# Performance work log

Hardware: AMD Instinct MI355X
Metric: run time of the kernel (lower is better)

The kernel has to match this reference:

```python
import jax, jax.numpy as jnp
import numpy as np

LN_EPS = 1e-5
SCALE = 1.0 / 8.0  # 1/sqrt(dim/num_heads) = 1/sqrt(64)


def layernorm(x, g, b):
    m = jnp.mean(x, axis=-1, keepdims=True)
    v = jnp.mean(jnp.square(x - m), axis=-1, keepdims=True)
    return (x - m) * jax.lax.rsqrt(v + LN_EPS) * g + b


def attention_block(q_in, kv_in, wq, bq, wk, bk, wv, bv, g, b):
    # un-split single-matrix attention, faithful to the source (no head reshape)
    Q = q_in @ wq + bq            # [B,S,D]
    K = kv_in @ wk + bk           # [B,T,D]
    V = kv_in @ wv + bv           # [B,T,D]
    scores = jnp.einsum('bsd,btd->bst', Q, K) * SCALE  # [B,S,T]
    A = jax.nn.softmax(scores, axis=-1)
    out = jnp.einsum('bst,btd->bsd', A, V)
    return layernorm(out + q_in, g, b)


def setup_inputs() -> dict:
    key = jax.random.key(0)
    ks = jax.random.split(key, 16)
    B, S, T, D = 4, 2048, 2048, 1024
    w = lambda k: jax.random.normal(k, (D, D), dtype=jnp.float32) * 0.02
    z = jnp.zeros((D,), dtype=jnp.float32)
    o = jnp.ones((D,), dtype=jnp.float32)
    return {
        'x': jax.random.normal(ks[0], (B, S, D), dtype=jnp.float32),
        'y': jax.random.normal(ks[1], (B, T, D), dtype=jnp.float32),
        'wq_m': w(ks[2]), 'bq_m': z, 'wk_m': w(ks[3]), 'bk_m': z,
        'wv_m': w(ks[4]), 'bv_m': z, 'g_m': o, 'b_m': z,
        'wq_c': w(ks[5]), 'bq_c': z, 'wk_c': w(ks[6]), 'bk_c': z,
        'wv_c': w(ks[7]), 'bv_c': z, 'g_c': o, 'b_c': z,
        'f0_w': w(ks[8]), 'f0_b': z, 'f1_w': w(ks[9]), 'f1_b': z,
        'g_d': o, 'b_d': z,
    }


def reference(x, y,
              wq_m, bq_m, wk_m, bk_m, wv_m, bv_m, g_m, b_m,
              wq_c, bq_c, wk_c, bk_c, wv_c, bv_c, g_c, b_c,
              f0_w, f0_b, f1_w, f1_b, g_d, b_d):
    # masked (self) attention + shared decoder LN residual
    res = x
    x = layernorm(attention_block(x, x, wq_m, bq_m, wk_m, bk_m, wv_m, bv_m, g_m, b_m) + res, g_d, b_d)
    # cross attention against memory y
    res = x
    x = layernorm(attention_block(x, y, wq_c, bq_c, wk_c, bk_c, wv_c, bv_c, g_c, b_c) + res, g_d, b_d)
    # FFN: loop condition in source is always true -> GELU (exact) after every layer
    res = x
    x = jax.nn.gelu(x @ f0_w + f0_b, approximate=False)
    x = jax.nn.gelu(x @ f1_w + f1_b, approximate=False)
    return layernorm(x + res, g_d, b_d)
```

## Files before the change

### kernel.cpp

```cpp
#include <hip/hip_runtime.h>

#define DEV __device__ __forceinline__

typedef __attribute__((ext_vector_type(8))) short bf16x8;
typedef __attribute__((ext_vector_type(4))) float f32x4;

DEV float bf2f(unsigned short u) { return __uint_as_float(((unsigned int)u) << 16); }
DEV unsigned short f2bf(float f) {
    unsigned int x = __float_as_uint(f);
    return (unsigned short)((x + 0x7fffu + ((x >> 16) & 1u)) >> 16);
}
DEV float gelu_exact(float x) { return 0.5f * x * (1.0f + erff(x * 0.7071067811865475f)); }

DEV void gload16(const void* g, void* l) {
    __builtin_amdgcn_global_load_lds((const __attribute__((address_space(1))) void*)g,
                                     (__attribute__((address_space(3))) void*)l, 16, 0, 0);
}

template <int OFF>
DEV bf16x8 ds_read128(unsigned addr) {
    bf16x8 r;
    asm volatile("ds_read_b128 %0, %1 offset:%2" : "=v"(r) : "v"(addr), "i"(OFF));
    return r;
}

struct WPtrs { const float* p[8]; };

__global__ __launch_bounds__(256) void transpose_cast_w8(WPtrs wp,
                                                         unsigned short* __restrict__ out,
                                                         int R, int C) {
    const float* in = wp.p[blockIdx.z];
    out += (size_t)blockIdx.z * R * C;
    __shared__ float tile[32][33];
    int c0 = blockIdx.x * 32, r0 = blockIdx.y * 32;
    int tx = threadIdx.x, ty = threadIdx.y;
#pragma unroll
    for (int i = 0; i < 32; i += 8)
        tile[ty + i][tx] = in[(size_t)(r0 + ty + i) * C + (c0 + tx)];
    __syncthreads();
#pragma unroll
    for (int i = 0; i < 32; i += 8)
        out[(size_t)(c0 + ty + i) * R + (r0 + tx)] = f2bf(tile[tx][ty + i]);
}

__global__ __launch_bounds__(256) void cast_f32_bf16(const float* __restrict__ in,
                                                     unsigned short* __restrict__ out, int n4) {
    int i = blockIdx.x * 256 + threadIdx.x;
    if (i >= n4) return;
    float4 v = ((const float4*)in)[i];
    unsigned short o[4] = {f2bf(v.x), f2bf(v.y), f2bf(v.z), f2bf(v.w)};
    *(uint2*)(out + (size_t)i * 4) = *(uint2*)o;
}


template <int H>
DEV void mfma16q(const bf16x8 (&a)[2][2], const bf16x8 (&b)[4][2], f32x4 (&acc)[4][4]) {
#pragma unroll
    for (int ks = 0; ks < 2; ++ks)
#pragma unroll
        for (int n = 0; n < 4; ++n) {
            acc[2 * H][n]     = __builtin_amdgcn_mfma_f32_16x16x32_bf16(a[0][ks], b[n][ks], acc[2 * H][n], 0, 0, 0);
            acc[2 * H + 1][n] = __builtin_amdgcn_mfma_f32_16x16x32_bf16(a[1][ks], b[n][ks], acc[2 * H + 1][n], 0, 0, 0);
        }
}

template <int BIAS_MODE, bool GELU_ACT, bool OUT_F32>
__global__ __launch_bounds__(256, 2) void gemm128(const unsigned short* __restrict__ A,
                                                  const unsigned short* __restrict__ BT,
                                                  const float* __restrict__ bias,
                                                  const float* __restrict__ biasB,
                                                  float* __restrict__ Cf,
                                                  unsigned short* __restrict__ Cb,
                                                  int N, int K, int lda, int ldb, float scale,
                                                  long sA, long sB, long sC) {
    const int gx = gridDim.x, gy = gridDim.y;
    int f = blockIdx.x + gx * (blockIdx.y + gy * blockIdx.z);
    const int nwg = gx * gy * gridDim.z;
    f = (f & 7) * (nwg >> 3) + (f >> 3);
    const int bz = f / (gx * gy);
    const int rem = f - bz * gx * gy;
    const int by = rem / gx;
    const int bx = rem - by * gx;

    A += (long)bz * sA;
    BT += (long)bz * sB;
    if (BIAS_MODE == 1 && biasB != nullptr && bz == 1) bias = biasB;

    const int tid = threadIdx.x;
    const int lane = tid & 63;
    const int wave = tid >> 6;
    const int wr = wave >> 1;
    const int wc = wave & 1;
    const int llo = lane & 15, lhi = lane >> 4;
    const int bm = bx * 128, bn = by * 128;

    __shared__ unsigned short lds[2][2][128 * 64];

    const int xk0 = (0 + lhi) ^ (llo & 7);
    const int xk1 = (4 + lhi) ^ (llo & 7);

    const unsigned base0 = (unsigned)(size_t)&lds[0][0][0];
    const unsigned aA0 = base0 + (unsigned)(wr * 64 + llo) * 128u + xk0 * 16;
    const unsigned aA1 = base0 + (unsigned)(wr * 64 + llo) * 128u + xk1 * 16;
    const unsigned aB0 = base0 + (unsigned)(wc * 64 + llo) * 128u + xk0 * 16;
    const unsigned aB1 = base0 + (unsigned)(wc * 64 + llo) * 128u + xk1 * 16;

    int srow[4], sq[4];
#pragma unroll
    for (int L = 0; L < 4; ++L) {
        const int d = L * 256 + tid;
        srow[L] = d >> 3;
        sq[L] = (d & 7) ^ (srow[L] & 7);
    }
    const unsigned short* gA = A + (size_t)bm * lda;
    const unsigned short* gB = BT + (size_t)bn * ldb;

#define SA(kt, BUF)                                                                     \
    {                                                                                   \
        _Pragma("unroll") for (int L = 0; L < 4; ++L)                                   \
            gload16(gA + (size_t)srow[L] * lda + (kt) + sq[L] * 8,                      \
                    &lds[BUF][0][(L * 256 + wave * 64) * 8]);                           \
    }
#define SB(kt, BUF)                                                                     \
    {                                                                                   \
        _Pragma("unroll") for (int L = 0; L < 4; ++L)                                   \
            gload16(gB + (size_t)srow[L] * ldb + (kt) + sq[L] * 8,                      \
                    &lds[BUF][1][(L * 256 + wave * 64) * 8]);                           \
    }

    f32x4 acc[4][4] = {};
    bf16x8 b[4][2];

#define PH(H, BUF, LOADB, STG, TAIL)                                         \
    {                                                                        \
        STG;                                                                 \
        bf16x8 afr[2][2];                                                    \
        afr[0][0] = ds_read128<(BUF)*32768 + (H)*4096 + 0>(aA0);             \
        afr[0][1] = ds_read128<(BUF)*32768 + (H)*4096 + 0>(aA1);             \
        afr[1][0] = ds_read128<(BUF)*32768 + (H)*4096 + 2048>(aA0);          \
        afr[1][1] = ds_read128<(BUF)*32768 + (H)*4096 + 2048>(aA1);          \
        if (LOADB) {                                                         \
            b[0][0] = ds_read128<(BUF)*32768 + 16384 + 0>(aB0);              \
            b[0][1] = ds_read128<(BUF)*32768 + 16384 + 0>(aB1);              \
            b[1][0] = ds_read128<(BUF)*32768 + 16384 + 2048>(aB0);           \
            b[1][1] = ds_read128<(BUF)*32768 + 16384 + 2048>(aB1);           \
            b[2][0] = ds_read128<(BUF)*32768 + 16384 + 4096>(aB0);           \
            b[2][1] = ds_read128<(BUF)*32768 + 16384 + 4096>(aB1);           \
            b[3][0] = ds_read128<(BUF)*32768 + 16384 + 6144>(aB0);           \
            b[3][1] = ds_read128<(BUF)*32768 + 16384 + 6144>(aB1);           \
        }                                                                    \
        __builtin_amdgcn_s_barrier();                                        \
        asm volatile("s_waitcnt lgkmcnt(0)" :::);                            \
        __builtin_amdgcn_sched_barrier(0);                                   \
        __builtin_amdgcn_s_setprio(1);                                       \
        mfma16q<H>(afr, b, acc);                                             \
        __builtin_amdgcn_s_setprio(0);                                       \
        TAIL;                                                                \
        __builtin_amdgcn_s_barrier();                                        \
    }

#define VM0 asm volatile("s_waitcnt vmcnt(0)" :::)
#define NOP ((void)0)

    const int nt = K >> 6;

    SA(0, 0);
    SB(0, 0);
    VM0;
    __builtin_amdgcn_s_barrier();

    int kt = 0;
    for (int t = 0; t < nt; t += 2) {
        const bool st0 = (t + 1 < nt);
        const bool st1 = (t + 2 < nt);
        PH(0, 0, true,  if (st0) { SA(kt + 64, 1); SB(kt + 64, 1); }, NOP);
        PH(1, 0, false, NOP, VM0);
        PH(0, 1, true,  if (st1) { SA(kt + 128, 0); SB(kt + 128, 0); }, NOP);
        PH(1, 1, false, NOP, VM0);
        kt += 128;
    }
#undef PH
#undef SA
#undef SB
#undef VM0
#undef NOP

#pragma unroll
    for (int m = 0; m < 4; ++m) {
#pragma unroll
        for (int n = 0; n < 4; ++n) {
            const int col = bn + wc * 64 + n * 16 + llo;
            float bcol = 0.f;
            if constexpr (BIAS_MODE == 1) bcol = bias[col];
#pragma unroll
            for (int j = 0; j < 4; ++j) {
                const int row = bm + wr * 64 + m * 16 + lhi * 4 + j;
                float v = acc[m][n][j] * scale + bcol;
                if constexpr (BIAS_MODE == 2) v += bias[row];
                if constexpr (GELU_ACT) v = gelu_exact(v);
                const size_t idx = (size_t)bz * (size_t)sC + (size_t)row * N + col;
                if constexpr (OUT_F32) Cf[idx] = v;
                else Cb[idx] = f2bf(v);
            }
        }
    }
}

__global__ __launch_bounds__(256) void softmax_rows(unsigned short* __restrict__ s, int T) {
    __shared__ float red[4];
    unsigned short* p = s + (size_t)blockIdx.x * T;
    const int tid = threadIdx.x;

    uint4 raw = *(const uint4*)(p + tid * 8);
    const unsigned short* u = (const unsigned short*)&raw;
    float v[8];
#pragma unroll
    for (int j = 0; j < 8; ++j) v[j] = bf2f(u[j]);

    float mx = -3.4e38f;
#pragma unroll
    for (int j = 0; j < 8; ++j) mx = fmaxf(mx, v[j]);
#pragma unroll
    for (int o = 32; o; o >>= 1) mx = fmaxf(mx, __shfl_xor(mx, o));
    if ((tid & 63) == 0) red[tid >> 6] = mx;
    __syncthreads();
    mx = fmaxf(fmaxf(red[0], red[1]), fmaxf(red[2], red[3]));
    __syncthreads();

    float sum = 0.f;
#pragma unroll
    for (int j = 0; j < 8; ++j) {
        v[j] = expf(v[j] - mx);
        sum += v[j];
    }
#pragma unroll
    for (int o = 32; o; o >>= 1) sum += __shfl_xor(sum, o);
    if ((tid & 63) == 0) red[tid >> 6] = sum;
    __syncthreads();
    sum = red[0] + red[1] + red[2] + red[3];
    const float inv = 1.0f / sum;

    unsigned short o8[8];
#pragma unroll
    for (int j = 0; j < 8; ++j) o8[j] = f2bf(v[j] * inv);
    *(uint4*)(p + tid * 8) = *(uint4*)o8;
}

DEV float block_sum(float v, float* red, int tid) {
#pragma unroll
    for (int o = 32; o; o >>= 1) v += __shfl_xor(v, o);
    if ((tid & 63) == 0) red[tid >> 6] = v;
    __syncthreads();
    v = red[0] + red[1] + red[2] + red[3];
    __syncthreads();
    return v;
}

__global__ __launch_bounds__(256) void ln_double(const unsigned short* __restrict__ av,
                                                 const float* __restrict__ xin,
                                                 const float* __restrict__ g1, const float* __restrict__ b1,
                                                 const float* __restrict__ g2, const float* __restrict__ b2,
                                                 float* __restrict__ xout,
                                                 unsigned short* __restrict__ xbf, int D) {
    __shared__ float red[4];
    const int tid = threadIdx.x;
    const size_t base = (size_t)blockIdx.x * D + tid * 4;
    uint2 a2 = *(const uint2*)(av + base);
    const unsigned short* au = (const unsigned short*)&a2;
    const float4 x4 = *(const float4*)(xin + base);
    float x[4] = {x4.x, x4.y, x4.z, x4.w};
    float t[4];
#pragma unroll
    for (int j = 0; j < 4; ++j) t[j] = bf2f(au[j]) + x[j];
    const float invD = 1.0f / D;

    float m = block_sum(t[0] + t[1] + t[2] + t[3], red, tid) * invD;
    float q = 0.f;
#pragma unroll
    for (int j = 0; j < 4; ++j) q += (t[j] - m) * (t[j] - m);
    q = block_sum(q, red, tid) * invD;
    float rs = rsqrtf(q + 1e-5f);

    float u[4];
#pragma unroll
    for (int j = 0; j < 4; ++j) {
        const int idx = tid * 4 + j;
        u[j] = (t[j] - m) * rs * g1[idx] + b1[idx] + x[j];
    }
    float m2 = block_sum(u[0] + u[1] + u[2] + u[3], red, tid) * invD;
    float q2 = 0.f;
#pragma unroll
    for (int j = 0; j < 4; ++j) q2 += (u[j] - m2) * (u[j] - m2);
    q2 = block_sum(q2, red, tid) * invD;
    float rs2 = rsqrtf(q2 + 1e-5f);

    float4 o4;
    unsigned short ob[4];
#pragma unroll
    for (int j = 0; j < 4; ++j) {
        const int idx = tid * 4 + j;
        float o = (u[j] - m2) * rs2 * g2[idx] + b2[idx];
        ((float*)&o4)[j] = o;
        ob[j] = f2bf(o);
    }
    *(float4*)(xout + base) = o4;
    *(uint2*)(xbf + base) = *(uint2*)ob;
}

__global__ __launch_bounds__(256) void ln_single(const unsigned short* __restrict__ a,
                                                 const float* __restrict__ b_,
                                                 const float* __restrict__ g, const float* __restrict__ bb,
                                                 float* __restrict__ out, int D) {
    __shared__ float red[4];
    const int tid = threadIdx.x;
    const size_t base = (size_t)blockIdx.x * D + tid * 4;
    uint2 a2 = *(const uint2*)(a + base);
    const unsigned short* au = (const unsigned short*)&a2;
    const float4 x4 = *(const float4*)(b_ + base);
    float t[4] = {bf2f(au[0]) + x4.x, bf2f(au[1]) + x4.y, bf2f(au[2]) + x4.z, bf2f(au[3]) + x4.w};
    const float invD = 1.0f / D;
    float m = block_sum(t[0] + t[1] + t[2] + t[3], red, tid) * invD;
    float q = 0.f;
#pragma unroll
    for (int j = 0; j < 4; ++j) q += (t[j] - m) * (t[j] - m);
    q = block_sum(q, red, tid) * invD;
    float rs = rsqrtf(q + 1e-5f);
    float4 o4;
#pragma unroll
    for (int j = 0; j < 4; ++j) {
        const int idx = tid * 4 + j;
        ((float*)&o4)[j] = (t[j] - m) * rs * g[idx] + bb[idx];
    }
    *(float4*)(out + base) = o4;
}

extern "C" void kernel_launch(void* const* d_in, const int* in_sizes, int n_in,
                              void* d_out, int out_size, void* d_ws, size_t ws_size,
                              hipStream_t stream) {
    (void)in_sizes; (void)n_in; (void)out_size; (void)ws_size;
    constexpr int B = 4, S = 2048, T = 2048, D = 1024;
    constexpr int M = B * S;
    constexpr long MD = (long)M * D;
    constexpr long ST = (long)S * T;
    constexpr long DD = (long)D * D;

    const float* x = (const float*)d_in[0];
    const float* y = (const float*)d_in[1];
    WPtrs wp;
    wp.p[0] = (const float*)d_in[2];
    wp.p[1] = (const float*)d_in[4];
    wp.p[2] = (const float*)d_in[6];
    wp.p[3] = (const float*)d_in[10];
    wp.p[4] = (const float*)d_in[12];
    wp.p[5] = (const float*)d_in[14];
    wp.p[6] = (const float*)d_in[18];
    wp.p[7] = (const float*)d_in[20];
    const float* bq_m = (const float*)d_in[3];
    const float* bk_m = (const float*)d_in[5];
    const float* bv_m = (const float*)d_in[7];
    const float* g_m = (const float*)d_in[8];
    const float* b_m = (const float*)d_in[9];
    const float* bq_c = (const float*)d_in[11];
    const float* bk_c = (const float*)d_in[13];
    const float* bv_c = (const float*)d_in[15];
    const float* g_c = (const float*)d_in[16];
    const float* b_c = (const float*)d_in[17];
    const float* f0_b = (const float*)d_in[19];
    const float* f1_b = (const float*)d_in[21];
    const float* g_d = (const float*)d_in[22];
    const float* b_d = (const float*)d_in[23];
    float* dout = (float*)d_out;

    char* p = (char*)d_ws;
    auto carve = [&](size_t bytes) { void* r = p; p += (bytes + 255) & ~(size_t)255; return r; };
    float* xcur = (float*)carve(MD * 4);
    unsigned short* wT = (unsigned short*)carve((size_t)8 * DD * 2);
    unsigned short* abf = (unsigned short*)carve(MD * 2);
    unsigned short* ybf = (unsigned short*)carve(MD * 2);
    unsigned short* Qb = (unsigned short*)carve(MD * 2);
    unsigned short* Kb = (unsigned short*)carve(MD * 2);
    unsigned short* Vt = (unsigned short*)carve(MD * 2);
    unsigned short* scores = (unsigned short*)carve((size_t)B * ST * 2);
    unsigned short* tmpb = (unsigned short*)carve(MD * 2);

    const dim3 blk256(256);
    const dim3 tb(32, 8);

    transpose_cast_w8<<<dim3(32, 32, 8), tb, 0, stream>>>(wp, wT, D, D);
    cast_f32_bf16<<<dim3(M * D / 4 / 256), blk256, 0, stream>>>(x, abf, M * D / 4);
    cast_f32_bf16<<<dim3(M * D / 4 / 256), blk256, 0, stream>>>(y, ybf, M * D / 4);

    unsigned short* wqm = wT + 0 * DD;
    unsigned short* wvm = wT + 2 * DD;
    unsigned short* wqc = wT + 3 * DD;
    unsigned short* wvc = wT + 5 * DD;
    unsigned short* wf0 = wT + 6 * DD;
    unsigned short* wf1 = wT + 7 * DD;

    const dim3 gQK(M / 128, D / 128, 2);
    const dim3 gVt(D / 128, T / 128, B);
    const dim3 gScores(S / 128, T / 128, B);
    const dim3 gPV(S / 128, D / 128, B);
    const dim3 gFFN(M / 128, D / 128, 1);

    gemm128<1, false, false><<<gQK, blk256, 0, stream>>>(abf, wqm, bq_m, bk_m, nullptr, Qb, D, D, D, D, 1.f, 0, DD, MD);
    gemm128<2, false, false><<<gVt, blk256, 0, stream>>>(wvm, abf, bv_m, nullptr, nullptr, Vt, T, D, D, D, 1.f, 0, (long)S * D, (long)D * T);
    gemm128<0, false, false><<<gScores, blk256, 0, stream>>>(Qb, Kb, nullptr, nullptr, nullptr, scores, T, D, D, D, 0.125f, (long)S * D, (long)T * D, ST);
    softmax_rows<<<dim3(B * S), blk256, 0, stream>>>(scores, T);
    gemm128<0, false, false><<<gPV, blk256, 0, stream>>>(scores, Vt, nullptr, nullptr, nullptr, tmpb, D, T, T, T, 1.f, ST, (long)T * D, (long)S * D);
    ln_double<<<dim3(M), blk256, 0, stream>>>(tmpb, x, g_m, b_m, g_d, b_d, xcur, abf, D);

    gemm128<1, false, false><<<gQK, blk256, 0, stream>>>(abf, wqc, bq_c, bk_c, nullptr, Qb, D, D, D, D, 1.f, MD, DD, MD);
    gemm128<2, false, false><<<gVt, blk256, 0, stream>>>(wvc, ybf, bv_c, nullptr, nullptr, Vt, T, D, D, D, 1.f, 0, (long)S * D, (long)D * T);
    gemm128<0, false, false><<<gScores, blk256, 0, stream>>>(Qb, Kb, nullptr, nullptr, nullptr, scores, T, D, D, D, 0.125f, (long)S * D, (long)T * D, ST);
    softmax_rows<<<dim3(B * S), blk256, 0, stream>>>(scores, T);
    gemm128<0, false, false><<<gPV, blk256, 0, stream>>>(scores, Vt, nullptr, nullptr, nullptr, tmpb, D, T, T, T, 1.f, ST, (long)T * D, (long)S * D);
    ln_double<<<dim3(M), blk256, 0, stream>>>(tmpb, xcur, g_c, b_c, g_d, b_d, xcur, abf, D);

    gemm128<1, true, false><<<gFFN, blk256, 0, stream>>>(abf, wf0, f0_b, nullptr, nullptr, Qb, D, D, D, D, 1.f, 0, 0, 0);
    gemm128<1, true, false><<<gFFN, blk256, 0, stream>>>(Qb, wf1, f1_b, nullptr, nullptr, tmpb, D, D, D, D, 1.f, 0, 0, 0);
    ln_single<<<dim3(M), blk256, 0, stream>>>(tmpb, xcur, g_d, b_d, dout, D);
}
```

Before: 462.2 us.

## Add 256x256-tile GEMM kernel for QK projection and score GEMMs

Introduces a new GEMM kernel with 256x256 output tiles per workgroup (each wave computing 128x128) and double-buffered LDS staging via global_load_lds. It is used for the fused Q/K projection and the attention score GEMMs to raise arithmetic intensity and cut global/LDS traffic per FLOP. The XCD block remapping is factored into a shared helper. In exchange, occupancy drops to one workgroup per CU, register pressure is very high (256 accumulators per thread), and the grids shrink to about one wave, so latency hiding and load balance may suffer.

```diff
diff --git a/kernel.cpp b/kernel.cpp
--- a/kernel.cpp
+++ b/kernel.cpp
@@ -52,6 +52,135 @@
     *(uint2*)(out + (size_t)i * 4) = *(uint2*)o;
 }
 
+DEV void xcd_remap(int& bx, int& by, int& bz) {
+    const int gx = gridDim.x, gy = gridDim.y;
+    int f = blockIdx.x + gx * (blockIdx.y + gy * blockIdx.z);
+    const int nwg = gx * gy * gridDim.z;
+    f = (f & 7) * (nwg >> 3) + (f >> 3);
+    bz = f / (gx * gy);
+    const int rem = f - bz * gx * gy;
+    by = rem / gx;
+    bx = rem - by * gx;
+}
+
+
+template <int BIAS_MODE>
+__global__ __launch_bounds__(256, 1) void gemm256x(const unsigned short* __restrict__ A,
+                                                   const unsigned short* __restrict__ BT,
+                                                   const float* __restrict__ bias,
+                                                   const float* __restrict__ biasB,
+                                                   unsigned short* __restrict__ Cb,
+                                                   int N, int K, int lda, int ldb, float scale,
+                                                   long sA, long sB, long sC) {
+    int bx, by, bz;
+    xcd_remap(bx, by, bz);
+    A += (long)bz * sA;
+    BT += (long)bz * sB;
+    if (BIAS_MODE == 1 && biasB != nullptr && bz == 1) bias = biasB;
+
+    const int tid = threadIdx.x;
+    const int lane = tid & 63;
+    const int wave = tid >> 6;
+    const int wm = wave >> 1;
+    const int wn = wave & 1;
+    const int llo = lane & 15, lhi = lane >> 4;
+    const int bm = bx * 256, bn = by * 256;
+
+    __shared__ unsigned short lds[2][2][256 * 64];
+
+    const int xk0 = (0 + lhi) ^ (llo & 7);
+    const int xk1 = (4 + lhi) ^ (llo & 7);
+
+    const unsigned base0 = (unsigned)(size_t)&lds[0][0][0];
+    const unsigned aA0 = base0 + (unsigned)(wm * 128 + llo) * 128u + xk0 * 16;
+    const unsigned aA1 = base0 + (unsigned)(wm * 128 + llo) * 128u + xk1 * 16;
+    const unsigned aB0 = base0 + 32768u + (unsigned)(wn * 128 + llo) * 128u + xk0 * 16;
+    const unsigned aB1 = base0 + 32768u + (unsigned)(wn * 128 + llo) * 128u + xk1 * 16;
+
+    const unsigned short* pA[8];
+    const unsigned short* pB[8];
+#pragma unroll
+    for (int L = 0; L < 8; ++L) {
+        const int d = L * 256 + tid;
+        const int r = d >> 3;
+        const int sc = ((d & 7) ^ (r & 7)) * 8;
+        pA[L] = A + (size_t)(bm + r) * lda + sc;
+        pB[L] = BT + (size_t)(bn + r) * ldb + sc;
+    }
+    const unsigned stW = (unsigned)wave * 1024u;
+    char* ldsc = (char*)&lds[0][0][0];
+
+#define STG(kt, BUF)                                                         \
+    {                                                                        \
+        _Pragma("unroll") for (int L = 0; L < 8; ++L)                        \
+            gload16(pA[L] + (kt), ldsc + (BUF)*65536 + L * 4096 + stW);      \
+        _Pragma("unroll") for (int L = 0; L < 8; ++L)                        \
+            gload16(pB[L] + (kt), ldsc + (BUF)*65536 + 32768 + L * 4096 + stW); \
+    }
+
+    f32x4 acc[8][8] = {};
+
+#define KS(CA, CB)                                                           \
+    {                                                                        \
+        bf16x8 af[8], bg[8];                                                 \
+        af[0] = ds_read128<0>(CA);      af[1] = ds_read128<2048>(CA);        \
+        af[2] = ds_read128<4096>(CA);   af[3] = ds_read128<6144>(CA);        \
+        af[4] = ds_read128<8192>(CA);   af[5] = ds_read128<10240>(CA);       \
+        af[6] = ds_read128<12288>(CA);  af[7] = ds_read128<14336>(CA);       \
+        bg[0] = ds_read128<0>(CB);      bg[1] = ds_read128<2048>(CB);        \
+        bg[2] = ds_read128<4096>(CB);   bg[3] = ds_read128<6144>(CB);        \
+        bg[4] = ds_read128<8192>(CB);   bg[5] = ds_read128<10240>(CB);       \
+        bg[6] = ds_read128<12288>(CB);  bg[7] = ds_read128<14336>(CB);       \
+        asm volatile("s_waitcnt lgkmcnt(0)" :::);                            \
+        __builtin_amdgcn_sched_barrier(0);                                   \
+        __builtin_amdgcn_s_setprio(1);                                       \
+        _Pragma("unroll") for (int m = 0; m < 8; ++m)                        \
+            _Pragma("unroll") for (int n = 0; n < 8; ++n)                    \
+                acc[m][n] = __builtin_amdgcn_mfma_f32_16x16x32_bf16(af[m], bg[n], acc[m][n], 0, 0, 0); \
+        __builtin_amdgcn_s_setprio(0);                                       \
+    }
+
+#define VM0 asm volatile("s_waitcnt vmcnt(0)" :::)
+
+    const int nt = K >> 6;
+
+    STG(0, 0);
+    VM0;
+    __builtin_amdgcn_s_barrier();
+
+    int kt = 64;
+    for (int t = 0; t < nt; ++t) {
+        const int buf = t & 1;
+        if (t + 1 < nt) {
+            if (buf == 0) STG(kt, 1) else STG(kt, 0);
+            kt += 64;
+        }
+        const unsigned bo = (unsigned)buf * 65536u;
+        KS(aA0 + bo, aB0 + bo);
+        KS(aA1 + bo, aB1 + bo);
+        VM0;
+        __builtin_amdgcn_s_barrier();
+    }
+#undef KS
+#undef STG
+#undef VM0
+
+#pragma unroll
+    for (int m = 0; m < 8; ++m) {
+#pragma unroll
+        for (int n = 0; n < 8; ++n) {
+            const int col = bn + wn * 128 + n * 16 + llo;
+            float bcol = 0.f;
+            if constexpr (BIAS_MODE == 1) bcol = bias[col];
+#pragma unroll
+            for (int j = 0; j < 4; ++j) {
+                const int row = bm + wm * 128 + m * 16 + lhi * 4 + j;
+                const size_t idx = (size_t)bz * (size_t)sC + (size_t)row * N + col;
+                Cb[idx] = f2bf(acc[m][n][j] * scale + bcol);
+            }
+        }
+    }
+}
 
 template <int H>
 DEV void mfma16q(const bf16x8 (&a)[2][2], const bf16x8 (&b)[4][2], f32x4 (&acc)[4][4]) {
@@ -73,15 +202,8 @@
                                                   unsigned short* __restrict__ Cb,
                                                   int N, int K, int lda, int ldb, float scale,
                                                   long sA, long sB, long sC) {
-    const int gx = gridDim.x, gy = gridDim.y;
-    int f = blockIdx.x + gx * (blockIdx.y + gy * blockIdx.z);
-    const int nwg = gx * gy * gridDim.z;
-    f = (f & 7) * (nwg >> 3) + (f >> 3);
-    const int bz = f / (gx * gy);
-    const int rem = f - bz * gx * gy;
-    const int by = rem / gx;
-    const int bx = rem - by * gx;
-
+    int bx, by, bz;
+    xcd_remap(bx, by, bz);
     A += (long)bz * sA;
     BT += (long)bz * sB;
     if (BIAS_MODE == 1 && biasB != nullptr && bz == 1) bias = biasB;
@@ -397,22 +519,22 @@
     unsigned short* wf0 = wT + 6 * DD;
     unsigned short* wf1 = wT + 7 * DD;
 
-    const dim3 gQK(M / 128, D / 128, 2);
+    const dim3 gQK(M / 256, D / 256, 2);
+    const dim3 gScores(S / 256, T / 256, B);
     const dim3 gVt(D / 128, T / 128, B);
-    const dim3 gScores(S / 128, T / 128, B);
     const dim3 gPV(S / 128, D / 128, B);
     const dim3 gFFN(M / 128, D / 128, 1);
 
-    gemm128<1, false, false><<<gQK, blk256, 0, stream>>>(abf, wqm, bq_m, bk_m, nullptr, Qb, D, D, D, D, 1.f, 0, DD, MD);
+    gemm256x<1><<<gQK, blk256, 0, stream>>>(abf, wqm, bq_m, bk_m, Qb, D, D, D, D, 1.f, 0, DD, MD);
     gemm128<2, false, false><<<gVt, blk256, 0, stream>>>(wvm, abf, bv_m, nullptr, nullptr, Vt, T, D, D, D, 1.f, 0, (long)S * D, (long)D * T);
-    gemm128<0, false, false><<<gScores, blk256, 0, stream>>>(Qb, Kb, nullptr, nullptr, nullptr, scores, T, D, D, D, 0.125f, (long)S * D, (long)T * D, ST);
+    gemm256x<0><<<gScores, blk256, 0, stream>>>(Qb, Kb, nullptr, nullptr, scores, T, D, D, D, 0.125f, (long)S * D, (long)T * D, ST);
     softmax_rows<<<dim3(B * S), blk256, 0, stream>>>(scores, T);
     gemm128<0, false, false><<<gPV, blk256, 0, stream>>>(scores, Vt, nullptr, nullptr, nullptr, tmpb, D, T, T, T, 1.f, ST, (long)T * D, (long)S * D);
     ln_double<<<dim3(M), blk256, 0, stream>>>(tmpb, x, g_m, b_m, g_d, b_d, xcur, abf, D);
 
-    gemm128<1, false, false><<<gQK, blk256, 0, stream>>>(abf, wqc, bq_c, bk_c, nullptr, Qb, D, D, D, D, 1.f, MD, DD, MD);
+    gemm256x<1><<<gQK, blk256, 0, stream>>>(abf, wqc, bq_c, bk_c, Qb, D, D, D, D, 1.f, MD, DD, MD);
     gemm128<2, false, false><<<gVt, blk256, 0, stream>>>(wvc, ybf, bv_c, nullptr, nullptr, Vt, T, D, D, D, 1.f, 0, (long)S * D, (long)D * T);
-    gemm128<0, false, false><<<gScores, blk256, 0, stream>>>(Qb, Kb, nullptr, nullptr, nullptr, scores, T, D, D, D, 0.125f, (long)S * D, (long)T * D, ST);
+    gemm256x<0><<<gScores, blk256, 0, stream>>>(Qb, Kb, nullptr, nullptr, scores, T, D, D, D, 0.125f, (long)S * D, (long)T * D, ST);
     softmax_rows<<<dim3(B * S), blk256, 0, stream>>>(scores, T);
     gemm128<0, false, false><<<gPV, blk256, 0, stream>>>(scores, Vt, nullptr, nullptr, nullptr, tmpb, D, T, T, T, 1.f, ST, (long)T * D, (long)S * D);
     ln_double<<<dim3(M), blk256, 0, stream>>>(tmpb, xcur, g_c, b_c, g_d, b_d, xcur, abf, D);
```

After: 476.4 us. +3.1%, slower.
